# Performance work log

Hardware: AMD Instinct MI355X
Metric: run time of the kernel (lower is better)

## Reference

```python
import jax, jax.numpy as jnp
import numpy as np

N_EMBD = 1024
N_HEAD = 16
B, T = 4, 2048


def setup_inputs() -> dict:
    key = jax.random.key(0)
    k1, k2, k3, k4, k5 = jax.random.split(key, 5)
    s = 0.02
    return {
        "x": jax.random.normal(k1, (B, T, N_EMBD), dtype=jnp.float32),
        "w_attn": jax.random.normal(k2, (N_EMBD, 3 * N_EMBD), dtype=jnp.float32) * s,
        "b_attn": jnp.zeros((3 * N_EMBD,), dtype=jnp.float32),
        "w_proj": jax.random.normal(k3, (N_EMBD, N_EMBD), dtype=jnp.float32) * s,
        "b_proj": jnp.zeros((N_EMBD,), dtype=jnp.float32),
    }


def reference(x, w_attn, b_attn, w_proj, b_proj):
    Bb, Tt, C = x.shape
    hd = C // N_HEAD  # head dim
    qkv = x @ w_attn + b_attn                      # [B,T,3C]
    q, k, v = jnp.split(qkv, 3, axis=-1)
    # [B,T,C] -> [B,H,T,hd]
    def heads(t):
        return t.reshape(Bb, Tt, N_HEAD, hd).transpose(0, 2, 1, 3)
    q, k, v = heads(q), heads(k), heads(v)
    scale = 1.0 / np.sqrt(hd).astype(np.float32)
    attn = jnp.einsum("bhqd,bhkd->bhqk", q, k) * scale  # [B,H,T,T]
    causal = jnp.tril(jnp.ones((Tt, Tt), dtype=bool))
    attn = jnp.where(causal, attn, -jnp.inf)
    attn = jax.nn.softmax(attn, axis=-1)
    y = jnp.einsum("bhqk,bhkd->bhqd", attn, v)          # [B,H,T,hd]
    y = y.transpose(0, 2, 1, 3).reshape(Bb, Tt, C)
    return y @ w_proj + b_proj
```

## Files before the change

kernel.cpp:

```cpp
#include <hip/hip_runtime.h>
#include <cmath>


typedef short short8 __attribute__((ext_vector_type(8)));
typedef short short4v __attribute__((ext_vector_type(4)));
typedef float f32x4 __attribute__((ext_vector_type(4)));

__device__ __forceinline__ short f2bf(float f) {
  unsigned u = __builtin_bit_cast(unsigned, f);
  u = (u + 0x7fffu + ((u >> 16) & 1u)) >> 16;
  return (short)u;
}

__device__ __forceinline__ float exp2_fast(float x) {
  float r;
  asm("v_exp_f32 %0, %1" : "=v"(r) : "v"(x));
  return r;
}

__device__ __forceinline__ void gld_lds16(const void* g, void* l) {
  __builtin_amdgcn_global_load_lds(
      (__attribute__((address_space(1))) void*)g,
      (__attribute__((address_space(3))) void*)l,
      16, 0, 0);
}

__global__ void cast_bf16_kernel(const float* __restrict__ in,
                                 short* __restrict__ out, int n4) {
  int i = blockIdx.x * blockDim.x + threadIdx.x;
  if (i < n4) {
    const float4 v = ((const float4*)in)[i];
    short4v o;
    o.x = f2bf(v.x); o.y = f2bf(v.y); o.z = f2bf(v.z); o.w = f2bf(v.w);
    ((short4v*)out)[i] = o;
  }
}

__global__ void transpose_cast_kernel(const float* __restrict__ in,
                                      short* __restrict__ out, int R, int C) {
  __shared__ float tile[32][33];
  int c0 = blockIdx.x * 32, r0 = blockIdx.y * 32;
  int tx = threadIdx.x & 31, tg = threadIdx.x >> 5;
#pragma unroll
  for (int i = 0; i < 4; ++i) {
    int r = tg * 4 + i;
    tile[r][tx] = in[(size_t)(r0 + r) * C + c0 + tx];
  }
  __syncthreads();
#pragma unroll
  for (int i = 0; i < 4; ++i) {
    int c = tg * 4 + i;
    out[(size_t)(c0 + c) * R + r0 + tx] = f2bf(tile[tx][c]);
  }
}

template <int MODE>
__global__ __launch_bounds__(256) void gemm_bt_kernel(
    const short* __restrict__ A, const short* __restrict__ Bt,
    const float* __restrict__ bias, float* __restrict__ outf,
    short* __restrict__ oq, short* __restrict__ ok, short* __restrict__ ovt,
    int M, int N, int K) {
  __shared__ short lds[(MODE == 0) ? 17408 : 16384];
  short* As = lds;
  short* Bs = lds + 8192;
  const int m0 = blockIdx.y * 128, n0 = blockIdx.x * 128;
  const int lane = threadIdx.x & 63, wave = threadIdx.x >> 6;
  const int quad = lane >> 4, l16 = lane & 15;
  const int wm = (wave >> 1) * 64, wn = (wave & 1) * 64;

  const int row_off = lane >> 3;
  const int segsw = ((lane & 7) ^ row_off) * 8;
  const short* Ag = A + (size_t)(m0 + wave * 32 + row_off) * K + segsw;
  const short* Bg = Bt + (size_t)(n0 + wave * 32 + row_off) * K + segsw;

  f32x4 acc[4][4] = {};

  for (int k0 = 0; k0 < K; k0 += 64) {
#pragma unroll
    for (int g = 0; g < 4; ++g) {
      gld_lds16(Ag + (size_t)(g * 8) * K + k0, &As[(wave * 32 + g * 8) * 64]);
      gld_lds16(Bg + (size_t)(g * 8) * K + k0, &Bs[(wave * 32 + g * 8) * 64]);
    }
    __syncthreads();
#pragma unroll
    for (int kh = 0; kh < 2; ++kh) {
      short8 a[4], b[4];
#pragma unroll
      for (int t = 0; t < 4; ++t) {
        const int R = wm + t * 16 + l16;
        a[t] = *(const short8*)&As[R * 64 + (((kh * 4 + quad) ^ (R & 7)) * 8)];
      }
#pragma unroll
      for (int t = 0; t < 4; ++t) {
        const int R = wn + t * 16 + l16;
        b[t] = *(const short8*)&Bs[R * 64 + (((kh * 4 + quad) ^ (R & 7)) * 8)];
      }
#pragma unroll
      for (int mt = 0; mt < 4; ++mt)
#pragma unroll
        for (int nt = 0; nt < 4; ++nt)
          acc[mt][nt] = __builtin_amdgcn_mfma_f32_16x16x32_bf16(
              a[mt], b[nt], acc[mt][nt], 0, 0, 0);
    }
    __syncthreads();
  }

  float bv[4];
#pragma unroll
  for (int nt = 0; nt < 4; ++nt) bv[nt] = bias[n0 + wn + nt * 16 + l16];

  if (MODE == 1) {
#pragma unroll
    for (int mt = 0; mt < 4; ++mt)
#pragma unroll
      for (int nt = 0; nt < 4; ++nt) {
        const int n = n0 + wn + nt * 16 + l16;
#pragma unroll
        for (int r = 0; r < 4; ++r) {
          const int m = m0 + wm + mt * 16 + quad * 4 + r;
          outf[(size_t)m * N + n] = acc[mt][nt][r] + bv[nt];
        }
      }
  } else {
    const int sec = n0 >> 10;
    short* Cs = lds;
    const float scale = (sec == 0) ? 0.18033688f : 1.0f;
#pragma unroll
    for (int mt = 0; mt < 4; ++mt)
#pragma unroll
      for (int nt = 0; nt < 4; ++nt) {
        const int col = wn + nt * 16 + l16;
#pragma unroll
        for (int r = 0; r < 4; ++r) {
          const int row = wm + mt * 16 + quad * 4 + r;
          const short h = f2bf((acc[mt][nt][r] + bv[nt]) * scale);
          if (sec == 2) Cs[col * 136 + row] = h;
          else          Cs[row * 136 + col] = h;
        }
      }
    __syncthreads();

    const int tid = threadIdx.x;
    const int rw = tid >> 1, half = tid & 1;
    const int h0 = (n0 & 1023) >> 6;
    const short* sp = &Cs[rw * 136 + half * 64];
    if (sec < 2) {
      short* dst = (sec == 0) ? oq : ok;
      const int m = m0 + rw, b_ = m >> 11, tt = m & 2047;
      short* gp = dst + ((size_t)(b_ * 16 + h0 + half) * 2048 + tt) * 64;
#pragma unroll
      for (int i = 0; i < 8; ++i) ((short8*)gp)[i] = ((const short8*)sp)[i];
    } else {
      const int b_ = m0 >> 11, t0 = m0 & 2047;
      const int bh = b_ * 16 + h0 + (rw >> 6), d = rw & 63;
      short* gp = ovt + ((size_t)bh * 64 + d) * 2048 + t0 + half * 64;
#pragma unroll
      for (int i = 0; i < 8; ++i) ((short8*)gp)[i] = ((const short8*)sp)[i];
    }
  }
}

__global__ __launch_bounds__(256, 6) void attn_kernel(
    const short* __restrict__ q, const short* __restrict__ k,
    const short* __restrict__ vt, short* __restrict__ y) {
  __shared__ short Ks[64 * 64];
  __shared__ short Vs[64 * 64];
  __shared__ short Ps[4][16 * 72];
  const int lane = threadIdx.x & 63, wave = threadIdx.x >> 6;
  const int quad = lane >> 4, l16 = lane & 15;
  const int g = blockIdx.x;
  const int bh = g & 63;
  const int j = 31 - (g >> 6);
  const int b_ = bh >> 4, h = bh & 15;
  const int q0 = j * 64 + wave * 16;

  const short* qbh = q + (size_t)bh * 2048 * 64;
  const short* kbh = k + (size_t)bh * 2048 * 64;
  const short* vbh = vt + (size_t)bh * 64 * 2048;
  short* Pw = Ps[wave];

  const short8 qf0 = *(const short8*)&qbh[(q0 + l16) * 64 + quad * 8];
  const short8 qf1 = *(const short8*)&qbh[(q0 + l16) * 64 + 32 + quad * 8];

  short8 ones;
#pragma unroll
  for (int i = 0; i < 8; ++i) ones[i] = (short)0x3F80;

  f32x4 O[4] = {};
  f32x4 lacc = {};

  const int srow = lane >> 3;
  const int scol = ((lane & 7) ^ srow) * 8;
  const int r0s = wave * 16;

#pragma unroll 1
  for (int c = 0; c <= j; ++c) {
    const int kt0 = c * 64;
    gld_lds16(kbh + (size_t)(kt0 + r0s + srow) * 64 + scol, &Ks[r0s * 64]);
    gld_lds16(kbh + (size_t)(kt0 + r0s + 8 + srow) * 64 + scol, &Ks[(r0s + 8) * 64]);
    gld_lds16(vbh + (size_t)(r0s + srow) * 2048 + kt0 + scol, &Vs[r0s * 64]);
    gld_lds16(vbh + (size_t)(r0s + 8 + srow) * 2048 + kt0 + scol, &Vs[(r0s + 8) * 64]);
    __syncthreads();

    const int sw = l16 & 7;
    f32x4 sc4[4];
#pragma unroll
    for (int cf = 0; cf < 4; ++cf) {
      const int row = cf * 16 + l16;
      const short8 kfa = *(const short8*)&Ks[row * 64 + ((quad ^ sw) * 8)];
      const short8 kfb = *(const short8*)&Ks[row * 64 + (((quad + 4) ^ sw) * 8)];
      f32x4 z = {};
      z = __builtin_amdgcn_mfma_f32_16x16x32_bf16(qf0, kfa, z, 0, 0, 0);
      z = __builtin_amdgcn_mfma_f32_16x16x32_bf16(qf1, kfb, z, 0, 0, 0);
      sc4[cf] = z;
    }

    if (c == j) {
#pragma unroll
      for (int cf = 0; cf < 4; ++cf) {
        const int col = kt0 + cf * 16 + l16;
#pragma unroll
        for (int r = 0; r < 4; ++r) {
          const int rowg = q0 + quad * 4 + r;
          float e = exp2_fast(sc4[cf][r]);
          e = (col > rowg) ? 0.f : e;
          Pw[(quad * 4 + r) * 72 + cf * 16 + l16] = f2bf(e);
        }
      }
    } else {
#pragma unroll
      for (int cf = 0; cf < 4; ++cf)
#pragma unroll
        for (int r = 0; r < 4; ++r)
          Pw[(quad * 4 + r) * 72 + cf * 16 + l16] = f2bf(exp2_fast(sc4[cf][r]));
    }
    asm volatile("s_waitcnt lgkmcnt(0)" ::: "memory");
    const short8 pf0 = *(const short8*)&Pw[l16 * 72 + quad * 8];
    const short8 pf1 = *(const short8*)&Pw[l16 * 72 + 32 + quad * 8];

    lacc = __builtin_amdgcn_mfma_f32_16x16x32_bf16(pf0, ones, lacc, 0, 0, 0);
    lacc = __builtin_amdgcn_mfma_f32_16x16x32_bf16(pf1, ones, lacc, 0, 0, 0);

#pragma unroll
    for (int dt = 0; dt < 4; ++dt) {
      const int d = dt * 16 + l16;
      const short8 vf0 = *(const short8*)&Vs[d * 64 + ((quad ^ sw) * 8)];
      const short8 vf1 = *(const short8*)&Vs[d * 64 + (((quad + 4) ^ sw) * 8)];
      O[dt] = __builtin_amdgcn_mfma_f32_16x16x32_bf16(pf0, vf0, O[dt], 0, 0, 0);
      O[dt] = __builtin_amdgcn_mfma_f32_16x16x32_bf16(pf1, vf1, O[dt], 0, 0, 0);
    }
    __syncthreads();
  }

  float inv[4];
#pragma unroll
  for (int r = 0; r < 4; ++r) inv[r] = 1.0f / lacc[r];
#pragma unroll
  for (int dt = 0; dt < 4; ++dt) {
    const int d = dt * 16 + l16;
#pragma unroll
    for (int r = 0; r < 4; ++r) {
      const int t_ = q0 + quad * 4 + r;
      y[((size_t)b_ * 2048 + t_) * 1024 + h * 64 + d] = f2bf(O[dt][r] * inv[r]);
    }
  }
}

extern "C" void kernel_launch(void* const* d_in, const int* in_sizes, int n_in,
                              void* d_out, int out_size, void* d_ws, size_t ws_size,
                              hipStream_t stream) {
  const float* x      = (const float*)d_in[0];
  const float* w_attn = (const float*)d_in[1];
  const float* b_attn = (const float*)d_in[2];
  const float* w_proj = (const float*)d_in[3];
  const float* b_proj = (const float*)d_in[4];
  float* out = (float*)d_out;

  short* xb  = (short*)d_ws;
  short* wTa = xb + (size_t)8192 * 1024;
  short* wTp = wTa + (size_t)3072 * 1024;
  short* qb  = wTp + (size_t)1024 * 1024;
  short* kb  = qb + (size_t)64 * 2048 * 64;
  short* vtb = kb + (size_t)64 * 2048 * 64;
  short* yb  = vtb + (size_t)64 * 2048 * 64;

  cast_bf16_kernel<<<8192, 256, 0, stream>>>(x, xb, 8192 * 1024 / 4);
  transpose_cast_kernel<<<dim3(96, 32), 256, 0, stream>>>(w_attn, wTa, 1024, 3072);
  transpose_cast_kernel<<<dim3(32, 32), 256, 0, stream>>>(w_proj, wTp, 1024, 1024);

  gemm_bt_kernel<0><<<dim3(24, 64), 256, 0, stream>>>(
      xb, wTa, b_attn, nullptr, qb, kb, vtb, 8192, 3072, 1024);

  attn_kernel<<<2048, 256, 0, stream>>>(qb, kb, vtb, yb);

  gemm_bt_kernel<1><<<dim3(8, 64), 256, 0, stream>>>(
      yb, wTp, b_proj, out, nullptr, nullptr, nullptr, 8192, 1024, 1024);
}
```

Baseline: 263.0 us.

## Enlarge attention query tile to 128 rows per block with balanced causal scheduling

Each attention block now handles 128 query rows (32 per wave, as two 16-row sub-tiles) instead of 64, so every K/V chunk staged in LDS feeds twice as many MFMAs and total K/V global traffic is halved. Blocks are ordered per head so that long and short causal tiles interleave (15,13,...,0,2,...), and waves skip chunks that lie entirely above their rows. Each wave now holds twice the accumulators, occupancy drops from 6 to 4 blocks per SIMD, and the grid shrinks to 1024 blocks. Waves also sit idle during the causal-diagonal chunks.

New measurement: 286.6 us. 9.0% more time.

```diff
diff --git a/kernel.cpp b/kernel.cpp
--- a/kernel.cpp
+++ b/kernel.cpp
@@ -160,41 +160,48 @@
   }
 }
 
-__global__ __launch_bounds__(256, 6) void attn_kernel(
+__global__ __launch_bounds__(256, 4) void attn_kernel(
     const short* __restrict__ q, const short* __restrict__ k,
     const short* __restrict__ vt, short* __restrict__ y) {
   __shared__ short Ks[64 * 64];
   __shared__ short Vs[64 * 64];
-  __shared__ short Ps[4][16 * 72];
+  __shared__ short Ps[4][32 * 72];
   const int lane = threadIdx.x & 63, wave = threadIdx.x >> 6;
   const int quad = lane >> 4, l16 = lane & 15;
   const int g = blockIdx.x;
-  const int bh = g & 63;
-  const int j = 31 - (g >> 6);
+  const int bh = g >> 4;
+  const int slot = g & 15;
+  const int jb = (slot < 8) ? (15 - 2 * slot) : (2 * slot - 16);
   const int b_ = bh >> 4, h = bh & 15;
-  const int q0 = j * 64 + wave * 16;
+  const int q0 = jb * 128 + wave * 32;
 
   const short* qbh = q + (size_t)bh * 2048 * 64;
   const short* kbh = k + (size_t)bh * 2048 * 64;
   const short* vbh = vt + (size_t)bh * 64 * 2048;
   short* Pw = Ps[wave];
 
-  const short8 qf0 = *(const short8*)&qbh[(q0 + l16) * 64 + quad * 8];
-  const short8 qf1 = *(const short8*)&qbh[(q0 + l16) * 64 + 32 + quad * 8];
+  short8 qf[2][2];
+#pragma unroll
+  for (int s = 0; s < 2; ++s) {
+    qf[s][0] = *(const short8*)&qbh[(q0 + s * 16 + l16) * 64 + quad * 8];
+    qf[s][1] = *(const short8*)&qbh[(q0 + s * 16 + l16) * 64 + 32 + quad * 8];
+  }
 
   short8 ones;
 #pragma unroll
   for (int i = 0; i < 8; ++i) ones[i] = (short)0x3F80;
 
-  f32x4 O[4] = {};
-  f32x4 lacc = {};
+  f32x4 O[2][4] = {};
+  f32x4 lacc[2] = {};
 
   const int srow = lane >> 3;
   const int scol = ((lane & 7) ^ srow) * 8;
   const int r0s = wave * 16;
+  const int sw = l16 & 7;
+  const int nch = 2 * jb + 2;
 
 #pragma unroll 1
-  for (int c = 0; c <= j; ++c) {
+  for (int c = 0; c < nch; ++c) {
     const int kt0 = c * 64;
     gld_lds16(kbh + (size_t)(kt0 + r0s + srow) * 64 + scol, &Ks[r0s * 64]);
     gld_lds16(kbh + (size_t)(kt0 + r0s + 8 + srow) * 64 + scol, &Ks[(r0s + 8) * 64]);
@@ -202,66 +209,91 @@
     gld_lds16(vbh + (size_t)(r0s + 8 + srow) * 2048 + kt0 + scol, &Vs[(r0s + 8) * 64]);
     __syncthreads();
 
-    const int sw = l16 & 7;
-    f32x4 sc4[4];
-#pragma unroll
-    for (int cf = 0; cf < 4; ++cf) {
-      const int row = cf * 16 + l16;
-      const short8 kfa = *(const short8*)&Ks[row * 64 + ((quad ^ sw) * 8)];
-      const short8 kfb = *(const short8*)&Ks[row * 64 + (((quad + 4) ^ sw) * 8)];
-      f32x4 z = {};
-      z = __builtin_amdgcn_mfma_f32_16x16x32_bf16(qf0, kfa, z, 0, 0, 0);
-      z = __builtin_amdgcn_mfma_f32_16x16x32_bf16(qf1, kfb, z, 0, 0, 0);
-      sc4[cf] = z;
-    }
-
-    if (c == j) {
+    if (kt0 < q0 + 32) {
+      f32x4 sc[2][4];
 #pragma unroll
       for (int cf = 0; cf < 4; ++cf) {
-        const int col = kt0 + cf * 16 + l16;
-#pragma unroll
-        for (int r = 0; r < 4; ++r) {
-          const int rowg = q0 + quad * 4 + r;
-          float e = exp2_fast(sc4[cf][r]);
-          e = (col > rowg) ? 0.f : e;
-          Pw[(quad * 4 + r) * 72 + cf * 16 + l16] = f2bf(e);
-        }
-      }
-    } else {
-#pragma unroll
-      for (int cf = 0; cf < 4; ++cf)
-#pragma unroll
-        for (int r = 0; r < 4; ++r)
-          Pw[(quad * 4 + r) * 72 + cf * 16 + l16] = f2bf(exp2_fast(sc4[cf][r]));
-    }
-    asm volatile("s_waitcnt lgkmcnt(0)" ::: "memory");
-    const short8 pf0 = *(const short8*)&Pw[l16 * 72 + quad * 8];
-    const short8 pf1 = *(const short8*)&Pw[l16 * 72 + 32 + quad * 8];
-
-    lacc = __builtin_amdgcn_mfma_f32_16x16x32_bf16(pf0, ones, lacc, 0, 0, 0);
-    lacc = __builtin_amdgcn_mfma_f32_16x16x32_bf16(pf1, ones, lacc, 0, 0, 0);
-
+        const int row = cf * 16 + l16;
+        const short8 kfa = *(const short8*)&Ks[row * 64 + ((quad ^ sw) * 8)];
+        const short8 kfb = *(const short8*)&Ks[row * 64 + (((quad + 4) ^ sw) * 8)];
+#pragma unroll
+        for (int s = 0; s < 2; ++s) {
+          f32x4 z = {};
+          z = __builtin_amdgcn_mfma_f32_16x16x32_bf16(qf[s][0], kfa, z, 0, 0, 0);
+          z = __builtin_amdgcn_mfma_f32_16x16x32_bf16(qf[s][1], kfb, z, 0, 0, 0);
+          sc[s][cf] = z;
+        }
+      }
+
+      if (kt0 + 64 > q0) {
+#pragma unroll
+        for (int s = 0; s < 2; ++s) {
+          const int qs = q0 + s * 16;
+#pragma unroll
+          for (int cf = 0; cf < 4; ++cf) {
+            const int col = kt0 + cf * 16 + l16;
+#pragma unroll
+            for (int r = 0; r < 4; ++r) {
+              const int rowg = qs + quad * 4 + r;
+              float e = exp2_fast(sc[s][cf][r]);
+              e = (col > rowg) ? 0.f : e;
+              Pw[(s * 16 + quad * 4 + r) * 72 + cf * 16 + l16] = f2bf(e);
+            }
+          }
+        }
+      } else {
+#pragma unroll
+        for (int s = 0; s < 2; ++s)
+#pragma unroll
+          for (int cf = 0; cf < 4; ++cf)
+#pragma unroll
+            for (int r = 0; r < 4; ++r)
+              Pw[(s * 16 + quad * 4 + r) * 72 + cf * 16 + l16] =
+                  f2bf(exp2_fast(sc[s][cf][r]));
+      }
+      asm volatile("s_waitcnt lgkmcnt(0)" ::: "memory");
+
+      short8 pf[2][2];
+#pragma unroll
+      for (int s = 0; s < 2; ++s) {
+        pf[s][0] = *(const short8*)&Pw[(s * 16 + l16) * 72 + quad * 8];
+        pf[s][1] = *(const short8*)&Pw[(s * 16 + l16) * 72 + 32 + quad * 8];
+      }
+
+#pragma unroll
+      for (int s = 0; s < 2; ++s) {
+        lacc[s] = __builtin_amdgcn_mfma_f32_16x16x32_bf16(pf[s][0], ones, lacc[s], 0, 0, 0);
+        lacc[s] = __builtin_amdgcn_mfma_f32_16x16x32_bf16(pf[s][1], ones, lacc[s], 0, 0, 0);
+      }
+
+#pragma unroll
+      for (int dt = 0; dt < 4; ++dt) {
+        const int d = dt * 16 + l16;
+        const short8 vf0 = *(const short8*)&Vs[d * 64 + ((quad ^ sw) * 8)];
+        const short8 vf1 = *(const short8*)&Vs[d * 64 + (((quad + 4) ^ sw) * 8)];
+#pragma unroll
+        for (int s = 0; s < 2; ++s) {
+          O[s][dt] = __builtin_amdgcn_mfma_f32_16x16x32_bf16(pf[s][0], vf0, O[s][dt], 0, 0, 0);
+          O[s][dt] = __builtin_amdgcn_mfma_f32_16x16x32_bf16(pf[s][1], vf1, O[s][dt], 0, 0, 0);
+        }
+      }
+    }
+    __syncthreads();
+  }
+
+#pragma unroll
+  for (int s = 0; s < 2; ++s) {
+    float inv[4];
+#pragma unroll
+    for (int r = 0; r < 4; ++r) inv[r] = 1.0f / lacc[s][r];
 #pragma unroll
     for (int dt = 0; dt < 4; ++dt) {
       const int d = dt * 16 + l16;
-      const short8 vf0 = *(const short8*)&Vs[d * 64 + ((quad ^ sw) * 8)];
-      const short8 vf1 = *(const short8*)&Vs[d * 64 + (((quad + 4) ^ sw) * 8)];
-      O[dt] = __builtin_amdgcn_mfma_f32_16x16x32_bf16(pf0, vf0, O[dt], 0, 0, 0);
-      O[dt] = __builtin_amdgcn_mfma_f32_16x16x32_bf16(pf1, vf1, O[dt], 0, 0, 0);
-    }
-    __syncthreads();
-  }
-
-  float inv[4];
-#pragma unroll
-  for (int r = 0; r < 4; ++r) inv[r] = 1.0f / lacc[r];
-#pragma unroll
-  for (int dt = 0; dt < 4; ++dt) {
-    const int d = dt * 16 + l16;
-#pragma unroll
-    for (int r = 0; r < 4; ++r) {
-      const int t_ = q0 + quad * 4 + r;
-      y[((size_t)b_ * 2048 + t_) * 1024 + h * 64 + d] = f2bf(O[dt][r] * inv[r]);
+#pragma unroll
+      for (int r = 0; r < 4; ++r) {
+        const int t_ = q0 + s * 16 + quad * 4 + r;
+        y[((size_t)b_ * 2048 + t_) * 1024 + h * 64 + d] = f2bf(O[s][dt][r] * inv[r]);
+      }
     }
   }
 }
@@ -291,7 +323,7 @@
   gemm_bt_kernel<0><<<dim3(24, 64), 256, 0, stream>>>(
       xb, wTa, b_attn, nullptr, qb, kb, vtb, 8192, 3072, 1024);
 
-  attn_kernel<<<2048, 256, 0, stream>>>(qb, kb, vtb, yb);
+  attn_kernel<<<1024, 256, 0, stream>>>(qb, kb, vtb, yb);
 
   gemm_bt_kernel<1><<<dim3(8, 64), 256, 0, stream>>>(
       yb, wTp, b_proj, out, nullptr, nullptr, nullptr, 8192, 1024, 1024);
```
